# Kernel optimization log

Hardware: AMD Instinct MI355X
Metric: run time of the kernel (lower is better)

The kernel has to match this reference:

```python
import jax, jax.numpy as jnp
import numpy as np

N_NODES = 50000
N_EDGES = 400000
N_GRAPHS = 128
IN_DIM = 768
HID = 128
N_CLASSES = 11
BN_EPS = 1e-5


def _sage_conv(x, src, dst, Wl, bl, Wr):
    # PyG SAGEConv (aggr='mean'): out = lin_l(mean_{j->i} x_j) + lin_r(x_i)
    # messages flow src -> dst; nodes with no in-edges get a zero aggregate.
    n = x.shape[0]
    deg = jax.ops.segment_sum(jnp.ones_like(dst, x.dtype), dst, num_segments=n)
    agg = jax.ops.segment_sum(x[src], dst, num_segments=n)  # [N, d] gather+scatter
    agg = agg / jnp.maximum(deg, 1.0)[:, None]
    return agg @ Wl.T + bl + x @ Wr.T


def _batch_norm(x, gamma, beta):
    # training-mode BatchNorm1d: biased batch statistics over the node axis
    m = jnp.mean(x, axis=0)
    v = jnp.var(x, axis=0)
    return (x - m) * jax.lax.rsqrt(v + BN_EPS) * gamma + beta


def setup_inputs() -> dict:
    key = jax.random.key(0)
    ks = jax.random.split(key, 16)
    x = jax.random.normal(ks[0], (N_NODES, IN_DIM), dtype=jnp.float32)
    edge_index = jax.random.randint(ks[1], (2, N_EDGES), 0, N_NODES, dtype=jnp.int32)
    batch = jnp.sort(jax.random.randint(ks[2], (N_NODES,), 0, N_GRAPHS, dtype=jnp.int32))

    def lin_w(k, out_d, in_d):
        return jax.random.normal(k, (out_d, in_d), dtype=jnp.float32) * (1.0 / np.sqrt(in_d))

    params = {
        'W1l': lin_w(ks[3], HID, IN_DIM), 'b1': jnp.zeros((HID,), jnp.float32),
        'W1r': lin_w(ks[4], HID, IN_DIM),
        'g1': jnp.ones((HID,), jnp.float32), 'be1': jnp.zeros((HID,), jnp.float32),
        'W2l': lin_w(ks[5], HID, HID), 'b2': jnp.zeros((HID,), jnp.float32),
        'W2r': lin_w(ks[6], HID, HID),
        'g2': jnp.ones((HID,), jnp.float32), 'be2': jnp.zeros((HID,), jnp.float32),
        'W3l': lin_w(ks[7], HID, HID), 'b3': jnp.zeros((HID,), jnp.float32),
        'W3r': lin_w(ks[8], HID, HID),
        'g3': jnp.ones((HID,), jnp.float32), 'be3': jnp.zeros((HID,), jnp.float32),
        'Wlin': lin_w(ks[9], N_CLASSES, HID), 'blin': jnp.zeros((N_CLASSES,), jnp.float32),
    }
    return {'x': x, 'edge_index': edge_index, 'batch': batch, **params}


def reference(x, edge_index, batch,
              W1l, b1, W1r, g1, be1,
              W2l, b2, W2r, g2, be2,
              W3l, b3, W3r, g3, be3,
              Wlin, blin):
    src, dst = edge_index[0], edge_index[1]
    h = jax.nn.relu(_batch_norm(_sage_conv(x, src, dst, W1l, b1, W1r), g1, be1))
    h = jax.nn.relu(_batch_norm(_sage_conv(h, src, dst, W2l, b2, W2r), g2, be2))
    h = _batch_norm(_sage_conv(h, src, dst, W3l, b3, W3r), g3, be3)
    # global_max_pool over graph ids
    pooled = jax.ops.segment_max(h, batch, num_segments=N_GRAPHS)  # [G, HID]
    # dropout is identity at inference
    return pooled @ Wlin.T + blin  # [G, 11]
```

## Files before the change

### kernel.cpp

```cpp
#include <hip/hip_runtime.h>

#define N_NODESC 50000
#define N_EDGESC 400000
#define N_GRAPHSC 128
#define IN_DIMC 768
#define HIDC 128
#define NCLSC 11
#define BN_EPSC 1e-5f
#define NB_AGG 8
#define NREP 64
#define SCAN_NB ((N_NODESC + 255) / 256)

typedef __bf16 bf16_t;
typedef __bf16 bf16x2 __attribute__((ext_vector_type(2)));
typedef __bf16 bf16x8 __attribute__((ext_vector_type(8)));
typedef float f32x4 __attribute__((ext_vector_type(4)));

typedef __attribute__((address_space(1))) void glb_void;
typedef __attribute__((address_space(3))) void lds_void;

__device__ __forceinline__ void cp16(const void* g, void* l) {
    __builtin_amdgcn_global_load_lds((glb_void*)g, (lds_void*)l, 16, 0, 0);
}

__device__ __forceinline__ f32x4 mfma_16x16x32_bf16(bf16x8 a, bf16x8 b, f32x4 c) {
    return __builtin_amdgcn_mfma_f32_16x16x32_bf16(a, b, c, 0, 0, 0);
}

template<int MODE, int KC>
__global__ __launch_bounds__(256) void gemm_kernel(const void* __restrict__ Av,
                                                   const bf16_t* __restrict__ Wb,
                                                   const float* __restrict__ stats,
                                                   const float* __restrict__ g,
                                                   const float* __restrict__ be,
                                                   bf16_t* __restrict__ Cl,
                                                   bf16_t* __restrict__ Cr,
                                                   int M)
{
    constexpr int NK   = KC / 32;
    constexpr int ASZ  = (MODE == 0) ? 16384 : 8192;
    constexpr int BSZ  = 8192;
    constexpr int NAB  = (MODE == 0) ? 2 : 3;
    constexpr int NBB  = (MODE == 0) ? 2 : 3;
    constexpr int AISS = (MODE == 0) ? 4 : 2;
    constexpr int AKB  = (MODE == 0) ? 128 : 64;
    constexpr int SCSZ = (MODE == 1) ? 1024 : 16;
    __shared__ __align__(16) unsigned char smem[NAB * ASZ + NBB * BSZ + SCSZ];
    unsigned char* Asm = smem;
    unsigned char* Bsm = smem + NAB * ASZ;
    float* scS = (float*)(smem + NAB * ASZ + NBB * BSZ);

    const int t    = threadIdx.x;
    const int m0   = blockIdx.x * 128;
    const int half = blockIdx.y;
    const int wid  = t >> 6;
    const int lane = t & 63;
    const int wm   = (wid >> 1) * 64;
    const int wn   = (wid & 1) * 64;
    const int l16  = lane & 15;
    const int quad = lane >> 4;

    const char* aSrc[AISS]; int aDst[AISS];
#pragma unroll
    for (int s = 0; s < AISS; s++) {
        int L = (s * 4 + wid) * 64 + lane;
        int r, c;
        if (MODE == 0) { r = L >> 3; c = (L & 7) ^ (r & 7); }
        else           { r = L >> 2; c = (L & 3) ^ ((r >> 1) & 3); }
        int row = m0 + r; if (row > M - 1) row = M - 1;
        if (MODE == 0) aSrc[s] = (const char*)Av + ((size_t)row * KC + (size_t)c * 4) * 4;
        else           aSrc[s] = (const char*)Av + ((size_t)row * KC + (size_t)c * 8) * 2;
        aDst[s] = (s * 4 + wid) * 1024;
    }
    const char* bSrc[2]; int bDst[2];
#pragma unroll
    for (int s = 0; s < 2; s++) {
        int L = (s * 4 + wid) * 64 + lane;
        int r = L >> 2;
        int c = (L & 3) ^ ((r >> 1) & 3);
        bSrc[s] = (const char*)(Wb + (size_t)(half * 128 + r) * KC + c * 8);
        bDst[s] = (s * 4 + wid) * 1024;
    }

    int aOff[4][2], bOff[4];
#pragma unroll
    for (int i = 0; i < 4; i++) {
        int ra = wm + i * 16 + l16;
        if (MODE == 0) {
            aOff[i][0] = ra * 128 + (((2 * quad)     ^ (ra & 7)) * 16);
            aOff[i][1] = ra * 128 + (((2 * quad + 1) ^ (ra & 7)) * 16);
        } else {
            aOff[i][0] = ra * 64 + ((quad ^ ((ra >> 1) & 3)) * 16);
            aOff[i][1] = 0;
        }
        int rb = wn + i * 16 + l16;
        bOff[i] = rb * 64 + ((quad ^ ((rb >> 1) & 3)) * 16);
    }

    if (MODE == 1) {
        if (t < HIDC) {
            float sum = 0.f, sumsq = 0.f;
            for (int r = 0; r < NREP; r++) {
                sum   += stats[r * 256 + t];
                sumsq += stats[r * 256 + HIDC + t];
            }
            float invM = 1.0f / (float)M;
            float mean = sum * invM;
            float var  = sumsq * invM - mean * mean;
            float s = rsqrtf(var + BN_EPSC) * g[t];
            scS[t] = s;
            scS[HIDC + t] = be[t] - mean * s;
        }
        __syncthreads();
    }

    f32x4 acc[4][4] = {};

    if constexpr (MODE == 0) {
#pragma unroll
        for (int s = 0; s < 4; s++) cp16(aSrc[s], Asm + aDst[s]);
#pragma unroll
        for (int s = 0; s < 2; s++) cp16(bSrc[s], Bsm + bDst[s]);

        for (int it = 0; it < NK; ++it) {
            if (it + 1 < NK) {
                const size_t ka = (size_t)(it + 1) * 128;
                const size_t kb = (size_t)(it + 1) * 64;
                const int nb = (it + 1) & 1;
#pragma unroll
                for (int s = 0; s < 4; s++) cp16(aSrc[s] + ka, Asm + nb * ASZ + aDst[s]);
#pragma unroll
                for (int s = 0; s < 2; s++) cp16(bSrc[s] + kb, Bsm + nb * BSZ + bDst[s]);
                asm volatile("s_waitcnt vmcnt(6)" ::: "memory");
            } else {
                asm volatile("s_waitcnt vmcnt(0)" ::: "memory");
            }
            asm volatile("s_barrier" ::: "memory");

            const unsigned char* Ab = Asm + (it & 1) * ASZ;
            const unsigned char* Bb = Bsm + (it & 1) * BSZ;
            bf16x8 af[4], bfr[4];
#pragma unroll
            for (int i = 0; i < 4; i++) {
                float4 u0 = *(const float4*)(Ab + aOff[i][0]);
                float4 u1 = *(const float4*)(Ab + aOff[i][1]);
                af[i][0] = (bf16_t)u0.x; af[i][1] = (bf16_t)u0.y;
                af[i][2] = (bf16_t)u0.z; af[i][3] = (bf16_t)u0.w;
                af[i][4] = (bf16_t)u1.x; af[i][5] = (bf16_t)u1.y;
                af[i][6] = (bf16_t)u1.z; af[i][7] = (bf16_t)u1.w;
            }
#pragma unroll
            for (int j = 0; j < 4; j++)
                bfr[j] = *(const bf16x8*)(Bb + bOff[j]);
#pragma unroll
            for (int i = 0; i < 4; i++)
#pragma unroll
                for (int j = 0; j < 4; j++)
                    acc[i][j] = mfma_16x16x32_bf16(af[i], bfr[j], acc[i][j]);

            asm volatile("s_barrier" ::: "memory");
        }
    } else {
#pragma unroll
        for (int s = 0; s < 2; s++) cp16(aSrc[s], Asm + aDst[s]);
#pragma unroll
        for (int s = 0; s < 2; s++) cp16(bSrc[s], Bsm + bDst[s]);
#pragma unroll
        for (int s = 0; s < 2; s++) cp16(aSrc[s] + 64, Asm + ASZ + aDst[s]);
#pragma unroll
        for (int s = 0; s < 2; s++) cp16(bSrc[s] + 64, Bsm + BSZ + bDst[s]);

        for (int it = 0; it < NK; ++it) {
            if (it + 2 < NK) {
                const size_t kb2 = (size_t)(it + 2) * 64;
                const int nb = (it + 2) % 3;
#pragma unroll
                for (int s = 0; s < 2; s++) cp16(aSrc[s] + kb2, Asm + nb * ASZ + aDst[s]);
#pragma unroll
                for (int s = 0; s < 2; s++) cp16(bSrc[s] + kb2, Bsm + nb * BSZ + bDst[s]);
                asm volatile("s_waitcnt vmcnt(8)" ::: "memory");
            } else if (it + 1 < NK) {
                asm volatile("s_waitcnt vmcnt(4)" ::: "memory");
            } else {
                asm volatile("s_waitcnt vmcnt(0)" ::: "memory");
            }
            asm volatile("s_barrier" ::: "memory");

            const unsigned char* Ab = Asm + (it % 3) * ASZ;
            const unsigned char* Bb = Bsm + (it % 3) * BSZ;
            bf16x8 af[4], bfr[4];
            float4 s0 = *(const float4*)&scS[it * 32 + quad * 8];
            float4 s1 = *(const float4*)&scS[it * 32 + quad * 8 + 4];
            float4 h0 = *(const float4*)&scS[HIDC + it * 32 + quad * 8];
            float4 h1 = *(const float4*)&scS[HIDC + it * 32 + quad * 8 + 4];
            float ss[8] = {s0.x, s0.y, s0.z, s0.w, s1.x, s1.y, s1.z, s1.w};
            float hh[8] = {h0.x, h0.y, h0.z, h0.w, h1.x, h1.y, h1.z, h1.w};
#pragma unroll
            for (int i = 0; i < 4; i++) {
                bf16x8 raw = *(const bf16x8*)(Ab + aOff[i][0]);
#pragma unroll
                for (int e = 0; e < 8; e++)
                    af[i][e] = (bf16_t)fmaxf(fmaf((float)raw[e], ss[e], hh[e]), 0.0f);
            }
#pragma unroll
            for (int j = 0; j < 4; j++)
                bfr[j] = *(const bf16x8*)(Bb + bOff[j]);
#pragma unroll
            for (int i = 0; i < 4; i++)
#pragma unroll
                for (int j = 0; j < 4; j++)
                    acc[i][j] = mfma_16x16x32_bf16(af[i], bfr[j], acc[i][j]);

            asm volatile("s_barrier" ::: "memory");
        }
    }

    bf16_t* C = half ? Cr : Cl;
#pragma unroll
    for (int i = 0; i < 4; i++) {
        int rowb = m0 + wm + i * 16 + quad * 4;
#pragma unroll
        for (int j = 0; j < 4; j++) {
            int colh = wn + j * 16 + l16;
#pragma unroll
            for (int rr = 0; rr < 4; rr++) {
                int row = rowb + rr;
                if (row < M) C[(size_t)row * HIDC + colh] = (bf16_t)acc[i][j][rr];
            }
        }
    }
}

__global__ void init_kernel(const float* __restrict__ W1l, const float* __restrict__ W1r,
                            const float* __restrict__ W2l, const float* __restrict__ W2r,
                            const float* __restrict__ W3l, const float* __restrict__ W3r,
                            bf16_t* __restrict__ Wb1, bf16_t* __restrict__ Wb2,
                            bf16_t* __restrict__ Wb3,
                            int* __restrict__ degi, float* __restrict__ stats)
{
    const int NW1 = 128 * IN_DIMC;
    const int NW2 = 128 * HIDC;
    const int NS  = 3 * NREP * 256;
    int j = blockIdx.x * blockDim.x + threadIdx.x;
    if (j < 2 * NW1) { Wb1[j] = (bf16_t)((j < NW1) ? W1l[j] : W1r[j - NW1]); return; }
    j -= 2 * NW1;
    if (j < 2 * NW2) { Wb2[j] = (bf16_t)((j < NW2) ? W2l[j] : W2r[j - NW2]); return; }
    j -= 2 * NW2;
    if (j < 2 * NW2) { Wb3[j] = (bf16_t)((j < NW2) ? W3l[j] : W3r[j - NW2]); return; }
    j -= 2 * NW2;
    if (j < NS) { stats[j] = 0.0f; return; }
    j -= NS;
    if (j < N_NODESC) degi[j] = 0;
}

__global__ void degi_kernel(const int* __restrict__ ei, int* __restrict__ degi) {
    int e = blockIdx.x * blockDim.x + threadIdx.x;
    if (e < N_EDGESC) atomicAdd(&degi[ei[N_EDGESC + e]], 1);
}

__global__ __launch_bounds__(256) void scan1_kernel(const int* __restrict__ degi,
                                                    int* __restrict__ local,
                                                    int* __restrict__ partials)
{
    __shared__ int tmp[256];
    const int t = threadIdx.x;
    const int i = blockIdx.x * 256 + t;
    int v = (i < N_NODESC) ? degi[i] : 0;
    tmp[t] = v;
    __syncthreads();
    for (int off = 1; off < 256; off <<= 1) {
        int u = (t >= off) ? tmp[t - off] : 0;
        __syncthreads();
        tmp[t] += u;
        __syncthreads();
    }
    if (i < N_NODESC) local[i] = tmp[t] - v;
    if (t == 255) partials[blockIdx.x] = tmp[255];
}

__global__ __launch_bounds__(256) void scan3_kernel(const int* __restrict__ local,
                                                    const int* __restrict__ partials,
                                                    int* __restrict__ rowptr,
                                                    int* __restrict__ cursor)
{
    __shared__ int inc[256];
    __shared__ int orig[256];
    const int t = threadIdx.x;
    int v = (t < SCAN_NB) ? partials[t] : 0;
    inc[t] = v; orig[t] = v;
    __syncthreads();
    for (int off = 1; off < 256; off <<= 1) {
        int u = (t >= off) ? inc[t - off] : 0;
        __syncthreads();
        inc[t] += u;
        __syncthreads();
    }
    const int boff = inc[blockIdx.x] - orig[blockIdx.x];
    const int i = blockIdx.x * 256 + t;
    if (i < N_NODESC) {
        int r = local[i] + boff;
        rowptr[i] = r;
        cursor[i] = r;
    }
    if (i == 0) rowptr[N_NODESC] = N_EDGESC;
}

__global__ void fill_kernel(const int* __restrict__ ei, int* __restrict__ cursor,
                            int* __restrict__ col) {
    int e = blockIdx.x * blockDim.x + threadIdx.x;
    if (e >= N_EDGESC) return;
    int d = ei[N_EDGESC + e];
    int pos = atomicAdd(&cursor[d], 1);
    col[pos] = ei[e];
}

__global__ __launch_bounds__(128) void agg_combine_kernel(const int* __restrict__ rowptr,
                                                          const int* __restrict__ col,
                                                          const bf16_t* __restrict__ Plb,
                                                          const bf16_t* __restrict__ Prb,
                                                          const float* __restrict__ bias,
                                                          bf16_t* __restrict__ Hb,
                                                          float* __restrict__ stats, int M)
{
    const int lane = threadIdx.x & 63;
    const int wv   = threadIdx.x >> 6;
    const int c0   = lane * 2;
    const float b0 = bias[c0], b1v = bias[c0 + 1];
    float s0 = 0.f, s1 = 0.f, q0 = 0.f, q1 = 0.f;
    const int n0 = blockIdx.x * NB_AGG + wv * (NB_AGG / 2);
    for (int rr = 0; rr < NB_AGG / 2; rr++) {
        int n = n0 + rr;
        if (n >= M) break;
        int lo = rowptr[n], hi = rowptr[n + 1];
        float a0 = 0.f, a1 = 0.f;
        for (int e = lo; e < hi; e += 8) {
            int rem = hi - e;
            int idx[8];
#pragma unroll
            for (int j = 0; j < 8; j++) {
                int ee = e + j; if (ee > hi - 1) ee = hi - 1;
                idx[j] = col[ee];
            }
            bf16x2 v[8];
#pragma unroll
            for (int j = 0; j < 8; j++)
                v[j] = *(const bf16x2*)&Plb[(size_t)idx[j] * HIDC + c0];
#pragma unroll
            for (int j = 0; j < 8; j++)
                if (j < rem) { a0 += (float)v[j][0]; a1 += (float)v[j][1]; }
        }
        int d = hi - lo;
        float inv = 1.0f / (float)(d > 0 ? d : 1);
        bf16x2 pr = *(const bf16x2*)&Prb[(size_t)n * HIDC + c0];
        float pre0 = fmaf(a0, inv, b0) + (float)pr[0];
        float pre1 = fmaf(a1, inv, b1v) + (float)pr[1];
        bf16x2 hv; hv[0] = (bf16_t)pre0; hv[1] = (bf16_t)pre1;
        *(bf16x2*)&Hb[(size_t)n * HIDC + c0] = hv;
        s0 += pre0; s1 += pre1; q0 += pre0 * pre0; q1 += pre1 * pre1;
    }
    const int rep = (blockIdx.x * 2 + wv) & (NREP - 1);
    atomicAdd(&stats[rep * 256 + c0], s0);
    atomicAdd(&stats[rep * 256 + c0 + 1], s1);
    atomicAdd(&stats[rep * 256 + HIDC + c0], q0);
    atomicAdd(&stats[rep * 256 + HIDC + c0 + 1], q1);
}

__global__ __launch_bounds__(128) void poolhead_kernel(const bf16_t* __restrict__ Hb,
                                                       const float* __restrict__ stats,
                                                       const float* __restrict__ g,
                                                       const float* __restrict__ be,
                                                       const int* __restrict__ batch,
                                                       const float* __restrict__ Wlin,
                                                       const float* __restrict__ blin,
                                                       float* __restrict__ out, int M)
{
    __shared__ float sp[HIDC];
    int gph = blockIdx.x;
    int c   = threadIdx.x;
    float sum = 0.f, sumsq = 0.f;
    for (int r = 0; r < NREP; r++) {
        sum   += stats[r * 256 + c];
        sumsq += stats[r * 256 + HIDC + c];
    }
    float invM = 1.0f / (float)M;
    float mean = sum * invM;
    float var  = sumsq * invM - mean * mean;
    float s = rsqrtf(var + BN_EPSC) * g[c];
    float h = be[c] - mean * s;

    int lo = 0, hi = M;
    while (lo < hi) { int m = (lo + hi) >> 1; if (batch[m] < gph) lo = m + 1; else hi = m; }
    int lo2 = lo, hi2 = M;
    while (lo2 < hi2) { int m = (lo2 + hi2) >> 1; if (batch[m] < gph + 1) lo2 = m + 1; else hi2 = m; }
    float mx = -INFINITY;
    for (int rr = lo; rr < lo2; rr++)
        mx = fmaxf(mx, fmaf((float)Hb[(size_t)rr * HIDC + c], s, h));
    sp[c] = mx;
    __syncthreads();
    if (c < NCLSC) {
        float acc = blin[c];
        for (int k = 0; k < HIDC; k++) acc += sp[k] * Wlin[c * HIDC + k];
        out[gph * NCLSC + c] = acc;
    }
}

extern "C" void kernel_launch(void* const* d_in, const int* in_sizes, int n_in,
                              void* d_out, int out_size, void* d_ws, size_t ws_size,
                              hipStream_t stream)
{
    const float* x     = (const float*)d_in[0];
    const int*   ei    = (const int*)d_in[1];
    const int*   batch = (const int*)d_in[2];
    const float* W1l = (const float*)d_in[3];
    const float* b1  = (const float*)d_in[4];
    const float* W1r = (const float*)d_in[5];
    const float* g1  = (const float*)d_in[6];
    const float* be1 = (const float*)d_in[7];
    const float* W2l = (const float*)d_in[8];
    const float* b2  = (const float*)d_in[9];
    const float* W2r = (const float*)d_in[10];
    const float* g2  = (const float*)d_in[11];
    const float* be2 = (const float*)d_in[12];
    const float* W3l = (const float*)d_in[13];
    const float* b3  = (const float*)d_in[14];
    const float* W3r = (const float*)d_in[15];
    const float* g3  = (const float*)d_in[16];
    const float* be3 = (const float*)d_in[17];
    const float* Wlin = (const float*)d_in[18];
    const float* blin = (const float*)d_in[19];

    const int M = N_NODESC;

    char* w = (char*)d_ws;
    bf16_t* Plb  = (bf16_t*)w;  w += (size_t)M * HIDC * 2;
    bf16_t* Prb  = (bf16_t*)w;  w += (size_t)M * HIDC * 2;
    bf16_t* Hb   = (bf16_t*)w;  w += (size_t)M * HIDC * 2;
    bf16_t* Wb1  = (bf16_t*)w;  w += (size_t)256 * IN_DIMC * 2;
    bf16_t* Wb2  = (bf16_t*)w;  w += (size_t)256 * HIDC * 2;
    bf16_t* Wb3  = (bf16_t*)w;  w += (size_t)256 * HIDC * 2;
    int*   rowptr= (int*)w;     w += (size_t)(M + 16) * 4;
    int*   col   = (int*)w;     w += (size_t)N_EDGESC * 4;
    int*   cursor= (int*)w;     w += (size_t)M * 4;
    int*   degi  = (int*)w;     w += (size_t)M * 4;
    int*   slocal= (int*)w;     w += (size_t)M * 4;
    int*   spart = (int*)w;     w += 256 * 4;
    float* stats = (float*)w;   w += (size_t)3 * NREP * 256 * 4;

    float* stats1 = stats;
    float* stats2 = stats + NREP * 256;
    float* stats3 = stats + 2 * NREP * 256;

    const dim3 gemm_grid((M + 127) / 128, 2);
    const int agg_blocks = (M + NB_AGG - 1) / NB_AGG;
    const int init_total = 2 * 128 * IN_DIMC + 4 * 128 * HIDC + 3 * NREP * 256 + M;

    init_kernel<<<(init_total + 255) / 256, 256, 0, stream>>>(W1l, W1r, W2l, W2r, W3l, W3r,
                                                              Wb1, Wb2, Wb3, degi, stats);
    degi_kernel<<<(N_EDGESC + 255) / 256, 256, 0, stream>>>(ei, degi);
    scan1_kernel<<<SCAN_NB, 256, 0, stream>>>(degi, slocal, spart);
    scan3_kernel<<<SCAN_NB, 256, 0, stream>>>(slocal, spart, rowptr, cursor);
    fill_kernel<<<(N_EDGESC + 255) / 256, 256, 0, stream>>>(ei, cursor, col);

    gemm_kernel<0, IN_DIMC><<<gemm_grid, 256, 0, stream>>>(x, Wb1, nullptr, nullptr, nullptr,
                                                           Plb, Prb, M);
    agg_combine_kernel<<<agg_blocks, 128, 0, stream>>>(rowptr, col, Plb, Prb, b1, Hb, stats1, M);

    gemm_kernel<1, HIDC><<<gemm_grid, 256, 0, stream>>>(Hb, Wb2, stats1, g1, be1, Plb, Prb, M);
    agg_combine_kernel<<<agg_blocks, 128, 0, stream>>>(rowptr, col, Plb, Prb, b2, Hb, stats2, M);

    gemm_kernel<1, HIDC><<<gemm_grid, 256, 0, stream>>>(Hb, Wb3, stats2, g2, be2, Plb, Prb, M);
    agg_combine_kernel<<<agg_blocks, 128, 0, stream>>>(rowptr, col, Plb, Prb, b3, Hb, stats3, M);

    poolhead_kernel<<<N_GRAPHSC, 128, 0, stream>>>(Hb, stats3, g3, be3, batch, Wlin, blin,
                                                   (float*)d_out, M);
}
```

Measured before the change: 574.5 us.

## Split GEMM kernels, load weights directly, single-shot small GEMM, per-node aggregation

```diff
diff --git a/kernel.cpp b/kernel.cpp
--- a/kernel.cpp
+++ b/kernel.cpp
@@ -7,7 +7,6 @@
 #define HIDC 128
 #define NCLSC 11
 #define BN_EPSC 1e-5f
-#define NB_AGG 8
 #define NREP 64
 #define SCAN_NB ((N_NODESC + 255) / 256)
 
@@ -27,28 +26,16 @@
     return __builtin_amdgcn_mfma_f32_16x16x32_bf16(a, b, c, 0, 0, 0);
 }
 
-template<int MODE, int KC>
-__global__ __launch_bounds__(256) void gemm_kernel(const void* __restrict__ Av,
-                                                   const bf16_t* __restrict__ Wb,
-                                                   const float* __restrict__ stats,
-                                                   const float* __restrict__ g,
-                                                   const float* __restrict__ be,
-                                                   bf16_t* __restrict__ Cl,
-                                                   bf16_t* __restrict__ Cr,
-                                                   int M)
-{
-    constexpr int NK   = KC / 32;
-    constexpr int ASZ  = (MODE == 0) ? 16384 : 8192;
-    constexpr int BSZ  = 8192;
-    constexpr int NAB  = (MODE == 0) ? 2 : 3;
-    constexpr int NBB  = (MODE == 0) ? 2 : 3;
-    constexpr int AISS = (MODE == 0) ? 4 : 2;
-    constexpr int AKB  = (MODE == 0) ? 128 : 64;
-    constexpr int SCSZ = (MODE == 1) ? 1024 : 16;
-    __shared__ __align__(16) unsigned char smem[NAB * ASZ + NBB * BSZ + SCSZ];
-    unsigned char* Asm = smem;
-    unsigned char* Bsm = smem + NAB * ASZ;
-    float* scS = (float*)(smem + NAB * ASZ + NBB * BSZ);
+__global__ __launch_bounds__(256) void gemm1_kernel(const float* __restrict__ A,
+                                                    const bf16_t* __restrict__ Wb,
+                                                    bf16_t* __restrict__ Cl,
+                                                    bf16_t* __restrict__ Cr,
+                                                    int M)
+{
+    constexpr int KC  = IN_DIMC;
+    constexpr int NK  = KC / 32;
+    constexpr int ASZ = 16384;
+    __shared__ __align__(16) unsigned char Asm[2 * ASZ];
 
     const int t    = threadIdx.x;
     const int m0   = blockIdx.x * 128;
@@ -60,159 +47,164 @@
     const int l16  = lane & 15;
     const int quad = lane >> 4;
 
-    const char* aSrc[AISS]; int aDst[AISS];
-#pragma unroll
-    for (int s = 0; s < AISS; s++) {
+    const char* aSrc[4]; int aDst[4];
+#pragma unroll
+    for (int s = 0; s < 4; s++) {
         int L = (s * 4 + wid) * 64 + lane;
-        int r, c;
-        if (MODE == 0) { r = L >> 3; c = (L & 7) ^ (r & 7); }
-        else           { r = L >> 2; c = (L & 3) ^ ((r >> 1) & 3); }
+        int r = L >> 3;
+        int c = (L & 7) ^ (r & 7);
         int row = m0 + r; if (row > M - 1) row = M - 1;
-        if (MODE == 0) aSrc[s] = (const char*)Av + ((size_t)row * KC + (size_t)c * 4) * 4;
-        else           aSrc[s] = (const char*)Av + ((size_t)row * KC + (size_t)c * 8) * 2;
+        aSrc[s] = (const char*)(A + (size_t)row * KC + c * 4);
         aDst[s] = (s * 4 + wid) * 1024;
     }
-    const char* bSrc[2]; int bDst[2];
-#pragma unroll
-    for (int s = 0; s < 2; s++) {
-        int L = (s * 4 + wid) * 64 + lane;
-        int r = L >> 2;
-        int c = (L & 3) ^ ((r >> 1) & 3);
-        bSrc[s] = (const char*)(Wb + (size_t)(half * 128 + r) * KC + c * 8);
-        bDst[s] = (s * 4 + wid) * 1024;
-    }
-
-    int aOff[4][2], bOff[4];
+    int aOff[4][2];
 #pragma unroll
     for (int i = 0; i < 4; i++) {
         int ra = wm + i * 16 + l16;
-        if (MODE == 0) {
-            aOff[i][0] = ra * 128 + (((2 * quad)     ^ (ra & 7)) * 16);
-            aOff[i][1] = ra * 128 + (((2 * quad + 1) ^ (ra & 7)) * 16);
+        aOff[i][0] = ra * 128 + (((2 * quad)     ^ (ra & 7)) * 16);
+        aOff[i][1] = ra * 128 + (((2 * quad + 1) ^ (ra & 7)) * 16);
+    }
+    const bf16_t* bB[4];
+#pragma unroll
+    for (int j = 0; j < 4; j++)
+        bB[j] = Wb + (size_t)(half * 128 + wn + j * 16 + l16) * KC + quad * 8;
+
+#pragma unroll
+    for (int s = 0; s < 4; s++) cp16(aSrc[s], Asm + aDst[s]);
+
+    f32x4 acc[4][4] = {};
+
+    for (int it = 0; it < NK; ++it) {
+        bf16x8 bfr[4];
+#pragma unroll
+        for (int j = 0; j < 4; j++)
+            bfr[j] = *(const bf16x8*)(bB[j] + it * 32);
+        asm volatile("" ::: "memory");
+        if (it + 1 < NK) {
+            const size_t ka = (size_t)(it + 1) * 128;
+            const int nb = (it + 1) & 1;
+#pragma unroll
+            for (int s = 0; s < 4; s++) cp16(aSrc[s] + ka, Asm + nb * ASZ + aDst[s]);
+            asm volatile("s_waitcnt vmcnt(4)" ::: "memory");
         } else {
-            aOff[i][0] = ra * 64 + ((quad ^ ((ra >> 1) & 3)) * 16);
-            aOff[i][1] = 0;
-        }
-        int rb = wn + i * 16 + l16;
-        bOff[i] = rb * 64 + ((quad ^ ((rb >> 1) & 3)) * 16);
-    }
-
-    if (MODE == 1) {
-        if (t < HIDC) {
-            float sum = 0.f, sumsq = 0.f;
-            for (int r = 0; r < NREP; r++) {
-                sum   += stats[r * 256 + t];
-                sumsq += stats[r * 256 + HIDC + t];
+            asm volatile("s_waitcnt vmcnt(0)" ::: "memory");
+        }
+        asm volatile("s_barrier" ::: "memory");
+
+        const unsigned char* Ab = Asm + (it & 1) * ASZ;
+        bf16x8 af[4];
+#pragma unroll
+        for (int i = 0; i < 4; i++) {
+            float4 u0 = *(const float4*)(Ab + aOff[i][0]);
+            float4 u1 = *(const float4*)(Ab + aOff[i][1]);
+            af[i][0] = (bf16_t)u0.x; af[i][1] = (bf16_t)u0.y;
+            af[i][2] = (bf16_t)u0.z; af[i][3] = (bf16_t)u0.w;
+            af[i][4] = (bf16_t)u1.x; af[i][5] = (bf16_t)u1.y;
+            af[i][6] = (bf16_t)u1.z; af[i][7] = (bf16_t)u1.w;
+        }
+#pragma unroll
+        for (int i = 0; i < 4; i++)
+#pragma unroll
+            for (int j = 0; j < 4; j++)
+                acc[i][j] = mfma_16x16x32_bf16(af[i], bfr[j], acc[i][j]);
+
+        asm volatile("s_barrier" ::: "memory");
+    }
+
+    bf16_t* C = half ? Cr : Cl;
+#pragma unroll
+    for (int i = 0; i < 4; i++) {
+        int rowb = m0 + wm + i * 16 + quad * 4;
+#pragma unroll
+        for (int j = 0; j < 4; j++) {
+            int colh = wn + j * 16 + l16;
+#pragma unroll
+            for (int rr = 0; rr < 4; rr++) {
+                int row = rowb + rr;
+                if (row < M) C[(size_t)row * HIDC + colh] = (bf16_t)acc[i][j][rr];
             }
-            float invM = 1.0f / (float)M;
-            float mean = sum * invM;
-            float var  = sumsq * invM - mean * mean;
-            float s = rsqrtf(var + BN_EPSC) * g[t];
-            scS[t] = s;
-            scS[HIDC + t] = be[t] - mean * s;
-        }
-        __syncthreads();
-    }
+        }
+    }
+}
+
+__global__ __launch_bounds__(256) void gemm23_kernel(const bf16_t* __restrict__ A,
+                                                     const bf16_t* __restrict__ Wb,
+                                                     const float* __restrict__ stats,
+                                                     const float* __restrict__ g,
+                                                     const float* __restrict__ be,
+                                                     bf16_t* __restrict__ Cl,
+                                                     bf16_t* __restrict__ Cr,
+                                                     int M)
+{
+    constexpr int KC = HIDC;
+    __shared__ __align__(16) unsigned char Asm[32768];
+    __shared__ __align__(16) unsigned char Bsm[32768];
+    __shared__ float scS[256];
+
+    const int t    = threadIdx.x;
+    const int m0   = blockIdx.x * 128;
+    const int half = blockIdx.y;
+    const int wid  = t >> 6;
+    const int lane = t & 63;
+    const int wm   = (wid >> 1) * 64;
+    const int wn   = (wid & 1) * 64;
+    const int l16  = lane & 15;
+    const int quad = lane >> 4;
+
+    if (t < HIDC) {
+        float sum = 0.f, sumsq = 0.f;
+        for (int r = 0; r < NREP; r++) {
+            sum   += stats[r * 256 + t];
+            sumsq += stats[r * 256 + HIDC + t];
+        }
+        float invM = 1.0f / (float)M;
+        float mean = sum * invM;
+        float var  = sumsq * invM - mean * mean;
+        float s = rsqrtf(var + BN_EPSC) * g[t];
+        scS[t] = s;
+        scS[HIDC + t] = be[t] - mean * s;
+    }
+
+#pragma unroll
+    for (int s = 0; s < 8; s++) {
+        int L = (s * 4 + wid) * 64 + lane;
+        int r = L >> 4;
+        int c = (L & 15) ^ (r & 7);
+        int row = m0 + r; if (row > M - 1) row = M - 1;
+        cp16((const char*)(A + (size_t)row * KC) + c * 16, Asm + (size_t)L * 16);
+        cp16((const char*)(Wb + (size_t)(half * 128 + r) * KC) + c * 16, Bsm + (size_t)L * 16);
+    }
+    __syncthreads();
 
     f32x4 acc[4][4] = {};
 
-    if constexpr (MODE == 0) {
-#pragma unroll
-        for (int s = 0; s < 4; s++) cp16(aSrc[s], Asm + aDst[s]);
-#pragma unroll
-        for (int s = 0; s < 2; s++) cp16(bSrc[s], Bsm + bDst[s]);
-
-        for (int it = 0; it < NK; ++it) {
-            if (it + 1 < NK) {
-                const size_t ka = (size_t)(it + 1) * 128;
-                const size_t kb = (size_t)(it + 1) * 64;
-                const int nb = (it + 1) & 1;
-#pragma unroll
-                for (int s = 0; s < 4; s++) cp16(aSrc[s] + ka, Asm + nb * ASZ + aDst[s]);
-#pragma unroll
-                for (int s = 0; s < 2; s++) cp16(bSrc[s] + kb, Bsm + nb * BSZ + bDst[s]);
-                asm volatile("s_waitcnt vmcnt(6)" ::: "memory");
-            } else {
-                asm volatile("s_waitcnt vmcnt(0)" ::: "memory");
-            }
-            asm volatile("s_barrier" ::: "memory");
-
-            const unsigned char* Ab = Asm + (it & 1) * ASZ;
-            const unsigned char* Bb = Bsm + (it & 1) * BSZ;
-            bf16x8 af[4], bfr[4];
-#pragma unroll
-            for (int i = 0; i < 4; i++) {
-                float4 u0 = *(const float4*)(Ab + aOff[i][0]);
-                float4 u1 = *(const float4*)(Ab + aOff[i][1]);
-                af[i][0] = (bf16_t)u0.x; af[i][1] = (bf16_t)u0.y;
-                af[i][2] = (bf16_t)u0.z; af[i][3] = (bf16_t)u0.w;
-                af[i][4] = (bf16_t)u1.x; af[i][5] = (bf16_t)u1.y;
-                af[i][6] = (bf16_t)u1.z; af[i][7] = (bf16_t)u1.w;
-            }
+#pragma unroll
+    for (int it = 0; it < KC / 32; ++it) {
+        bf16x8 af[4], bfr[4];
+        float4 s0 = *(const float4*)&scS[it * 32 + quad * 8];
+        float4 s1 = *(const float4*)&scS[it * 32 + quad * 8 + 4];
+        float4 h0 = *(const float4*)&scS[HIDC + it * 32 + quad * 8];
+        float4 h1 = *(const float4*)&scS[HIDC + it * 32 + quad * 8 + 4];
+        float ss[8] = {s0.x, s0.y, s0.z, s0.w, s1.x, s1.y, s1.z, s1.w};
+        float hh[8] = {h0.x, h0.y, h0.z, h0.w, h1.x, h1.y, h1.z, h1.w};
+#pragma unroll
+        for (int i = 0; i < 4; i++) {
+            int ra = wm + i * 16 + l16;
+            bf16x8 raw = *(const bf16x8*)(Asm + ra * 256 + (((it * 4 + quad) ^ (ra & 7)) * 16));
+#pragma unroll
+            for (int e = 0; e < 8; e++)
+                af[i][e] = (bf16_t)fmaxf(fmaf((float)raw[e], ss[e], hh[e]), 0.0f);
+        }
+#pragma unroll
+        for (int j = 0; j < 4; j++) {
+            int rb = wn + j * 16 + l16;
+            bfr[j] = *(const bf16x8*)(Bsm + rb * 256 + (((it * 4 + quad) ^ (rb & 7)) * 16));
+        }
+#pragma unroll
+        for (int i = 0; i < 4; i++)
 #pragma unroll
             for (int j = 0; j < 4; j++)
-                bfr[j] = *(const bf16x8*)(Bb + bOff[j]);
-#pragma unroll
-            for (int i = 0; i < 4; i++)
-#pragma unroll
-                for (int j = 0; j < 4; j++)
-                    acc[i][j] = mfma_16x16x32_bf16(af[i], bfr[j], acc[i][j]);
-
-            asm volatile("s_barrier" ::: "memory");
-        }
-    } else {
-#pragma unroll
-        for (int s = 0; s < 2; s++) cp16(aSrc[s], Asm + aDst[s]);
-#pragma unroll
-        for (int s = 0; s < 2; s++) cp16(bSrc[s], Bsm + bDst[s]);
-#pragma unroll
-        for (int s = 0; s < 2; s++) cp16(aSrc[s] + 64, Asm + ASZ + aDst[s]);
-#pragma unroll
-        for (int s = 0; s < 2; s++) cp16(bSrc[s] + 64, Bsm + BSZ + bDst[s]);
-
-        for (int it = 0; it < NK; ++it) {
-            if (it + 2 < NK) {
-                const size_t kb2 = (size_t)(it + 2) * 64;
-                const int nb = (it + 2) % 3;
-#pragma unroll
-                for (int s = 0; s < 2; s++) cp16(aSrc[s] + kb2, Asm + nb * ASZ + aDst[s]);
-#pragma unroll
-                for (int s = 0; s < 2; s++) cp16(bSrc[s] + kb2, Bsm + nb * BSZ + bDst[s]);
-                asm volatile("s_waitcnt vmcnt(8)" ::: "memory");
-            } else if (it + 1 < NK) {
-                asm volatile("s_waitcnt vmcnt(4)" ::: "memory");
-            } else {
-                asm volatile("s_waitcnt vmcnt(0)" ::: "memory");
-            }
-            asm volatile("s_barrier" ::: "memory");
-
-            const unsigned char* Ab = Asm + (it % 3) * ASZ;
-            const unsigned char* Bb = Bsm + (it % 3) * BSZ;
-            bf16x8 af[4], bfr[4];
-            float4 s0 = *(const float4*)&scS[it * 32 + quad * 8];
-            float4 s1 = *(const float4*)&scS[it * 32 + quad * 8 + 4];
-            float4 h0 = *(const float4*)&scS[HIDC + it * 32 + quad * 8];
-            float4 h1 = *(const float4*)&scS[HIDC + it * 32 + quad * 8 + 4];
-            float ss[8] = {s0.x, s0.y, s0.z, s0.w, s1.x, s1.y, s1.z, s1.w};
-            float hh[8] = {h0.x, h0.y, h0.z, h0.w, h1.x, h1.y, h1.z, h1.w};
-#pragma unroll
-            for (int i = 0; i < 4; i++) {
-                bf16x8 raw = *(const bf16x8*)(Ab + aOff[i][0]);
-#pragma unroll
-                for (int e = 0; e < 8; e++)
-                    af[i][e] = (bf16_t)fmaxf(fmaf((float)raw[e], ss[e], hh[e]), 0.0f);
-            }
-#pragma unroll
-            for (int j = 0; j < 4; j++)
-                bfr[j] = *(const bf16x8*)(Bb + bOff[j]);
-#pragma unroll
-            for (int i = 0; i < 4; i++)
-#pragma unroll
-                for (int j = 0; j < 4; j++)
-                    acc[i][j] = mfma_16x16x32_bf16(af[i], bfr[j], acc[i][j]);
-
-            asm volatile("s_barrier" ::: "memory");
-        }
+                acc[i][j] = mfma_16x16x32_bf16(af[i], bfr[j], acc[i][j]);
     }
 
     bf16_t* C = half ? Cr : Cl;
@@ -314,7 +306,7 @@
     col[pos] = ei[e];
 }
 
-__global__ __launch_bounds__(128) void agg_combine_kernel(const int* __restrict__ rowptr,
+__global__ __launch_bounds__(256) void agg_combine_kernel(const int* __restrict__ rowptr,
                                                           const int* __restrict__ col,
                                                           const bf16_t* __restrict__ Plb,
                                                           const bf16_t* __restrict__ Prb,
@@ -325,44 +317,40 @@
     const int lane = threadIdx.x & 63;
     const int wv   = threadIdx.x >> 6;
     const int c0   = lane * 2;
-    const float b0 = bias[c0], b1v = bias[c0 + 1];
-    float s0 = 0.f, s1 = 0.f, q0 = 0.f, q1 = 0.f;
-    const int n0 = blockIdx.x * NB_AGG + wv * (NB_AGG / 2);
-    for (int rr = 0; rr < NB_AGG / 2; rr++) {
-        int n = n0 + rr;
-        if (n >= M) break;
-        int lo = rowptr[n], hi = rowptr[n + 1];
-        float a0 = 0.f, a1 = 0.f;
-        for (int e = lo; e < hi; e += 8) {
-            int rem = hi - e;
-            int idx[8];
-#pragma unroll
-            for (int j = 0; j < 8; j++) {
-                int ee = e + j; if (ee > hi - 1) ee = hi - 1;
-                idx[j] = col[ee];
-            }
-            bf16x2 v[8];
-#pragma unroll
-            for (int j = 0; j < 8; j++)
-                v[j] = *(const bf16x2*)&Plb[(size_t)idx[j] * HIDC + c0];
-#pragma unroll
-            for (int j = 0; j < 8; j++)
-                if (j < rem) { a0 += (float)v[j][0]; a1 += (float)v[j][1]; }
-        }
-        int d = hi - lo;
-        float inv = 1.0f / (float)(d > 0 ? d : 1);
-        bf16x2 pr = *(const bf16x2*)&Prb[(size_t)n * HIDC + c0];
-        float pre0 = fmaf(a0, inv, b0) + (float)pr[0];
-        float pre1 = fmaf(a1, inv, b1v) + (float)pr[1];
-        bf16x2 hv; hv[0] = (bf16_t)pre0; hv[1] = (bf16_t)pre1;
-        *(bf16x2*)&Hb[(size_t)n * HIDC + c0] = hv;
-        s0 += pre0; s1 += pre1; q0 += pre0 * pre0; q1 += pre1 * pre1;
-    }
-    const int rep = (blockIdx.x * 2 + wv) & (NREP - 1);
-    atomicAdd(&stats[rep * 256 + c0], s0);
-    atomicAdd(&stats[rep * 256 + c0 + 1], s1);
-    atomicAdd(&stats[rep * 256 + HIDC + c0], q0);
-    atomicAdd(&stats[rep * 256 + HIDC + c0 + 1], q1);
+    const int n    = blockIdx.x * 4 + wv;
+    if (n >= M) return;
+
+    int lo = rowptr[n], hi = rowptr[n + 1];
+    float a0 = 0.f, a1 = 0.f;
+    for (int e = lo; e < hi; e += 8) {
+        int rem = hi - e;
+        int idx[8];
+#pragma unroll
+        for (int j = 0; j < 8; j++) {
+            int ee = e + j; if (ee > hi - 1) ee = hi - 1;
+            idx[j] = col[ee];
+        }
+        bf16x2 v[8];
+#pragma unroll
+        for (int j = 0; j < 8; j++)
+            v[j] = *(const bf16x2*)&Plb[(size_t)idx[j] * HIDC + c0];
+#pragma unroll
+        for (int j = 0; j < 8; j++)
+            if (j < rem) { a0 += (float)v[j][0]; a1 += (float)v[j][1]; }
+    }
+    int d = hi - lo;
+    float inv = 1.0f / (float)(d > 0 ? d : 1);
+    bf16x2 pr = *(const bf16x2*)&Prb[(size_t)n * HIDC + c0];
+    float pre0 = fmaf(a0, inv, bias[c0]) + (float)pr[0];
+    float pre1 = fmaf(a1, inv, bias[c0 + 1]) + (float)pr[1];
+    bf16x2 hv; hv[0] = (bf16_t)pre0; hv[1] = (bf16_t)pre1;
+    *(bf16x2*)&Hb[(size_t)n * HIDC + c0] = hv;
+
+    const int rep = n & (NREP - 1);
+    atomicAdd(&stats[rep * 256 + c0], pre0);
+    atomicAdd(&stats[rep * 256 + c0 + 1], pre1);
+    atomicAdd(&stats[rep * 256 + HIDC + c0], pre0 * pre0);
+    atomicAdd(&stats[rep * 256 + HIDC + c0 + 1], pre1 * pre1);
 }
 
 __global__ __launch_bounds__(128) void poolhead_kernel(const bf16_t* __restrict__ Hb,
@@ -451,7 +439,7 @@
     float* stats3 = stats + 2 * NREP * 256;
 
     const dim3 gemm_grid((M + 127) / 128, 2);
-    const int agg_blocks = (M + NB_AGG - 1) / NB_AGG;
+    const int agg_blocks = (M + 3) / 4;
     const int init_total = 2 * 128 * IN_DIMC + 4 * 128 * HIDC + 3 * NREP * 256 + M;
 
     init_kernel<<<(init_total + 255) / 256, 256, 0, stream>>>(W1l, W1r, W2l, W2r, W3l, W3r,
@@ -461,15 +449,14 @@
     scan3_kernel<<<SCAN_NB, 256, 0, stream>>>(slocal, spart, rowptr, cursor);
     fill_kernel<<<(N_EDGESC + 255) / 256, 256, 0, stream>>>(ei, cursor, col);
 
-    gemm_kernel<0, IN_DIMC><<<gemm_grid, 256, 0, stream>>>(x, Wb1, nullptr, nullptr, nullptr,
-                                                           Plb, Prb, M);
-    agg_combine_kernel<<<agg_blocks, 128, 0, stream>>>(rowptr, col, Plb, Prb, b1, Hb, stats1, M);
-
-    gemm_kernel<1, HIDC><<<gemm_grid, 256, 0, stream>>>(Hb, Wb2, stats1, g1, be1, Plb, Prb, M);
-    agg_combine_kernel<<<agg_blocks, 128, 0, stream>>>(rowptr, col, Plb, Prb, b2, Hb, stats2, M);
-
-    gemm_kernel<1, HIDC><<<gemm_grid, 256, 0, stream>>>(Hb, Wb3, stats2, g2, be2, Plb, Prb, M);
-    agg_combine_kernel<<<agg_blocks, 128, 0, stream>>>(rowptr, col, Plb, Prb, b3, Hb, stats3, M);
+    gemm1_kernel<<<gemm_grid, 256, 0, stream>>>(x, Wb1, Plb, Prb, M);
+    agg_combine_kernel<<<agg_blocks, 256, 0, stream>>>(rowptr, col, Plb, Prb, b1, Hb, stats1, M);
+
+    gemm23_kernel<<<gemm_grid, 256, 0, stream>>>(Hb, Wb2, stats1, g1, be1, Plb, Prb, M);
+    agg_combine_kernel<<<agg_blocks, 256, 0, stream>>>(rowptr, col, Plb, Prb, b2, Hb, stats2, M);
+
+    gemm23_kernel<<<gemm_grid, 256, 0, stream>>>(Hb, Wb3, stats2, g2, be2, Plb, Prb, M);
+    agg_combine_kernel<<<agg_blocks, 256, 0, stream>>>(rowptr, col, Plb, Prb, b3, Hb, stats3, M);
 
     poolhead_kernel<<<N_GRAPHSC, 128, 0, stream>>>(Hb, stats3, g3, be3, batch, Wlin, blin,
                                                    (float*)d_out, M);
```

After: 802.2 us. 1.4x slower.
